# Kernel tuning notes

Hardware: AMD Instinct MI355X
Metric: run time of the kernel (lower is better)

The kernel has to match this reference:

```python
import jax, jax.numpy as jnp
import numpy as np

B, S, D, DEPTH = 2, 2048, 1024, 4
NUM_LEAVES = 2 ** DEPTH          # 16
NUM_DEC = NUM_LEAVES - 1         # 15


def setup_inputs() -> dict:
    key = jax.random.key(0)
    k1, k2, k3, k4, k5 = jax.random.split(key, 5)
    scale = 1.0 / np.sqrt(D)
    return {
        "x": jax.random.normal(k1, (B, S, D), dtype=jnp.float32),
        "dec_w": jax.random.normal(k2, (NUM_DEC, D), dtype=jnp.float32) * scale,
        "dec_b": jax.random.normal(k3, (NUM_DEC,), dtype=jnp.float32) * scale,
        "leaf_w": jax.random.normal(k4, (NUM_LEAVES, D, D), dtype=jnp.float32) * scale,  # [leaf, out, in] (torch Linear layout)
        "leaf_b": jax.random.normal(k5, (NUM_LEAVES, D), dtype=jnp.float32) * scale,
    }


def reference(x, dec_w, dec_b, leaf_w, leaf_b):
    num_leaves = leaf_w.shape[0]
    num_dec = num_leaves - 1
    # All decision-node sigmoids in one batched GEMM: [B,S,num_dec]
    dec = jax.nn.sigmoid(jnp.einsum("bsd,nd->bsn", x, dec_w) + dec_b)
    # Faithful to the original: each tree slot is multiplied exactly once by its
    # direct parent's decision (left child: p, right child: 1-p).
    leaf_idx = np.arange(num_dec, 2 * num_leaves - 1)      # slots holding leaf probs
    parent = (leaf_idx - 1) // 2                           # [num_leaves]
    is_left = (leaf_idx % 2 == 1)                          # [num_leaves]
    dec_p = dec[..., parent]                               # [B,S,num_leaves]
    leaf_probs = jnp.where(jnp.asarray(is_left), dec_p, 1.0 - dec_p)
    # All leaf MLPs as one batched GEMM: [B,S,L,D]
    leaf_out = jnp.einsum("bsd,lod->bslo", x, leaf_w) + leaf_b
    # Probability-weighted sum over leaves -> [B,S,D]
    return jnp.einsum("bslo,bsl->bso", leaf_out, leaf_probs)
```

## Files before the change

kernel.cpp:

```cpp
#include <hip/hip_runtime.h>
#include <stdint.h>


#define M_TOK 4096
#define DDIM  1024
#define KFLAT 9216

typedef __bf16 bf16x8 __attribute__((ext_vector_type(8)));
typedef float  f32x4  __attribute__((ext_vector_type(4)));
typedef unsigned short u16x4 __attribute__((ext_vector_type(4)));
typedef unsigned short u16x8 __attribute__((ext_vector_type(8)));

#define GLB(p) ((const __attribute__((address_space(1))) void*)(p))
#define LDS(p) ((__attribute__((address_space(3))) void*)(p))

__device__ __forceinline__ unsigned short f2bf(float f) {
    union { float f; uint32_t u; } v; v.f = f;
    uint32_t u = v.u;
    return (unsigned short)((u + 0x7fffu + ((u >> 16) & 1u)) >> 16);
}

__device__ __forceinline__ bf16x8 asbf(f32x4 v) {
    bf16x8 r; __builtin_memcpy(&r, &v, 16); return r;
}

template<int OFF>
__device__ __forceinline__ f32x4 dsr(uint32_t a) {
    f32x4 r;
    asm volatile("ds_read_b128 %0, %1 offset:%c2" : "=v"(r) : "v"(a), "i"(OFF));
    return r;
}

__global__ __launch_bounds__(256) void prep_dec_kernel(
    const float* __restrict__ x, const float* __restrict__ dec_w,
    const float* __restrict__ dec_b, const float* __restrict__ lw,
    const float* __restrict__ lb, unsigned short* __restrict__ wp,
    float* __restrict__ bw, unsigned short* __restrict__ xs,
    float* __restrict__ pmat)
{
    if (blockIdx.x < 1024) {
        int idx = blockIdx.x * 256 + threadIdx.x;
        int o  = idx >> 8;
        int k4 = (idx & 255) << 2;
        size_t src = (size_t)o * DDIM + k4;
        size_t dstb = (size_t)o * KFLAT + k4;
        float4 acc = make_float4(0.f, 0.f, 0.f, 0.f);
#pragma unroll
        for (int j = 0; j < 8; ++j) {
            const float4 a = *(const float4*)(lw + (size_t)(2*j)   * DDIM*DDIM + src);
            const float4 b = *(const float4*)(lw + (size_t)(2*j+1) * DDIM*DDIM + src);
            u16x4 d;
            d[0] = f2bf(a.x - b.x); d[1] = f2bf(a.y - b.y);
            d[2] = f2bf(a.z - b.z); d[3] = f2bf(a.w - b.w);
            *(u16x4*)(wp + dstb + (size_t)j * DDIM) = d;
            acc.x += b.x; acc.y += b.y; acc.z += b.z; acc.w += b.w;
        }
        u16x4 s;
        s[0] = f2bf(acc.x); s[1] = f2bf(acc.y); s[2] = f2bf(acc.z); s[3] = f2bf(acc.w);
        *(u16x4*)(wp + dstb + (size_t)8 * DDIM) = s;
        if ((idx & 255) == 0) {
            float sb = 0.f;
#pragma unroll
            for (int j = 0; j < 8; ++j) {
                float ba = lb[(2*j) * DDIM + o];
                float bb = lb[(2*j+1) * DDIM + o];
                bw[j * DDIM + o] = ba - bb;
                sb += bb;
            }
            bw[8 * DDIM + o] = sb;
        }
    } else {
        int m    = (blockIdx.x - 1024) * 4 + (threadIdx.x >> 6);
        int lane = threadIdx.x & 63;
        const float* xr = x + (size_t)m * DDIM + lane * 16;
        float xv[16];
        *(float4*)&xv[0]  = *(const float4*)(xr + 0);
        *(float4*)&xv[4]  = *(const float4*)(xr + 4);
        *(float4*)&xv[8]  = *(const float4*)(xr + 8);
        *(float4*)&xv[12] = *(const float4*)(xr + 12);
        float s[8];
#pragma unroll
        for (int j = 0; j < 8; ++j) {
            const float* wr = dec_w + (size_t)(7 + j) * DDIM + lane * 16;
            float a = 0.f;
#pragma unroll
            for (int i = 0; i < 16; i += 4) {
                float4 wv = *(const float4*)(wr + i);
                a = fmaf(xv[i], wv.x, fmaf(xv[i+1], wv.y, fmaf(xv[i+2], wv.z, fmaf(xv[i+3], wv.w, a))));
            }
            s[j] = a;
        }
#pragma unroll
        for (int j = 0; j < 8; ++j)
#pragma unroll
            for (int off = 32; off > 0; off >>= 1)
                s[j] += __shfl_xor(s[j], off);
        float p[8];
#pragma unroll
        for (int j = 0; j < 8; ++j)
            p[j] = 1.0f / (1.0f + expf(-(s[j] + dec_b[7 + j])));
        if (lane == 0) {
#pragma unroll
            for (int j = 0; j < 8; ++j)
                pmat[(size_t)m * 8 + j] = p[j];
        }
#pragma unroll
        for (int j = 0; j < 9; ++j) {
            float pj = (j < 8) ? p[j] : 1.0f;
            unsigned short* dst = xs + (size_t)m * KFLAT + j * DDIM + lane * 16;
#pragma unroll
            for (int c = 0; c < 2; ++c) {
                u16x8 o;
#pragma unroll
                for (int e = 0; e < 8; ++e) o[e] = f2bf(pj * xv[c * 8 + e]);
                *(u16x8*)(dst + c * 8) = o;
            }
        }
    }
}

#define WAITV0 asm volatile("s_waitcnt vmcnt(0)" ::: "memory")
#define WAITV4 asm volatile("s_waitcnt vmcnt(4)" ::: "memory")
#define WAITV8 asm volatile("s_waitcnt vmcnt(8)" ::: "memory")
#define BARR   __builtin_amdgcn_s_barrier()
#define SBAR   __builtin_amdgcn_sched_barrier(0)
#define LGKM0  do { asm volatile("s_waitcnt lgkmcnt(0)" ::: "memory"); SBAR; } while(0)
#define LGKM4  do { asm volatile("s_waitcnt lgkmcnt(4)" ::: "memory"); SBAR; } while(0)

#define MFMA_Q(q, ASET, BSET) do { \
    __builtin_amdgcn_s_setprio(1); \
    _Pragma("unroll") \
    for (int mfl = 0; mfl < 2; ++mfl) { \
        _Pragma("unroll") \
        for (int j = 0; j < 4; ++j) { \
            acc[2*(q)+mfl][j] = __builtin_amdgcn_mfma_f32_16x16x32_bf16(asbf(ASET[mfl][0]), asbf(BSET[j][0]), acc[2*(q)+mfl][j], 0, 0, 0); \
            acc[2*(q)+mfl][j] = __builtin_amdgcn_mfma_f32_16x16x32_bf16(asbf(ASET[mfl][1]), asbf(BSET[j][1]), acc[2*(q)+mfl][j], 0, 0, 0); \
        } \
    } \
    __builtin_amdgcn_s_setprio(0); \
} while(0)

#define READ_A(SET, q, a0, a1) do { \
    SET[0][0] = dsr<(2*(q)+0)*2048>(a0); \
    SET[0][1] = dsr<(2*(q)+0)*2048>(a1); \
    SET[1][0] = dsr<(2*(q)+1)*2048>(a0); \
    SET[1][1] = dsr<(2*(q)+1)*2048>(a1); \
} while(0)

#define READ_B(SET, b0, b1) do { \
    SET[0][0] = dsr<0*2048>(b0); SET[0][1] = dsr<0*2048>(b1); \
    SET[1][0] = dsr<1*2048>(b0); SET[1][1] = dsr<1*2048>(b1); \
    SET[2][0] = dsr<2*2048>(b0); SET[2][1] = dsr<2*2048>(b1); \
    SET[3][0] = dsr<3*2048>(b0); SET[3][1] = dsr<3*2048>(b1); \
} while(0)

__global__ __launch_bounds__(512, 2) void tree_gemm8(
    const unsigned short* __restrict__ xs, const unsigned short* __restrict__ wp,
    float* __restrict__ out, float* __restrict__ parts, int KG)
{
    extern __shared__ char smem[];
    const int tid  = threadIdx.x;
    const int lane = tid & 63;
    const int w    = tid >> 6;
    const int wm   = w >> 2, wn = w & 3;
    const int ra   = lane & 15;
    const int g16  = lane >> 4;

    const int bx  = blockIdx.x;
    const int xcd = bx & 7, ii = bx >> 3;
    const int nt  = xcd >> 1;
    const int mt  = (xcd & 1) * 8 + ii;
    const int m0  = mt * 256, n0 = nt * 256;
    const int g   = blockIdx.y;
    const int k0  = g * KG;
    const int NT  = KG >> 6;

    uint32_t sbase = (uint32_t)(uintptr_t)(__attribute__((address_space(3))) char*)smem;
    const uint32_t colb0 = (uint32_t)((g16 ^ (ra & 7)) << 4);
    const uint32_t colb1 = colb0 ^ 64;
    const uint32_t baseA0s = sbase + wm * 16384 + ra * 128 + colb0;
    const uint32_t baseA1s = sbase + wm * 16384 + ra * 128 + colb1;
    const uint32_t baseB0s = sbase + 65536 + wn * 8192 + ra * 128 + colb0;
    const uint32_t baseB1s = sbase + 65536 + wn * 8192 + ra * 128 + colb1;

    const int kel = (((lane & 7) ^ (lane >> 3)) & 7) * 8;
    const int rA  = w * 8 + (lane >> 3);

    auto stageA = [&](int buf, int tt, int hh) {
        const unsigned short* s0 = xs + (size_t)(m0 + hh * 128 + rA) * KFLAT + (k0 + tt * 64 + kel);
        char* d0 = smem + buf * 32768 + hh * 16384 + w * 1024;
        __builtin_amdgcn_global_load_lds(GLB(s0), LDS(d0), 16, 0, 0);
        __builtin_amdgcn_global_load_lds(GLB(s0 + (size_t)64 * KFLAT), LDS(d0 + 8192), 16, 0, 0);
    };
    auto stageB = [&](int buf, int tt, int hh) {
        const unsigned short* s0 = wp + (size_t)(n0 + hh * 128 + rA) * KFLAT + (k0 + tt * 64 + kel);
        char* d0 = smem + 65536 + buf * 32768 + hh * 16384 + w * 1024;
        __builtin_amdgcn_global_load_lds(GLB(s0), LDS(d0), 16, 0, 0);
        __builtin_amdgcn_global_load_lds(GLB(s0 + (size_t)64 * KFLAT), LDS(d0 + 8192), 16, 0, 0);
    };

    f32x4 acc[8][4] = {};
    f32x4 avA[2][2], avB[2][2], bvX[4][2], bvY[4][2];

    stageA(0, 0, 0); stageA(0, 0, 1);
    stageB(0, 0, 0); stageB(0, 0, 1);
    stageB(1, 1, 0); stageB(1, 1, 1);
    WAITV4;
    BARR;
    READ_B(bvX, baseB0s, baseB1s);
    READ_A(avA, 0, baseA0s, baseA1s);

    int bt1 = 1, bt2 = 2;

#define TILE_BODY(T, CUR, NXT) do { \
    const int t_ = (T); \
    const bool s1 = (t_ + 1 < NT), s2 = (t_ + 2 < NT); \
    if (s1) { stageA((t_ + 1) & 1, t_ + 1, 0); stageA((t_ + 1) & 1, t_ + 1, 1); } \
    if (s2) { stageB(bt2, t_ + 2, 0); stageB(bt2, t_ + 2, 1); } \
    const uint32_t a0_ = baseA0s + ((uint32_t)(t_ & 1) << 15); \
    const uint32_t a1_ = baseA1s + ((uint32_t)(t_ & 1) << 15); \
    READ_A(avB, 1, a0_, a1_); \
    LGKM4;  MFMA_Q(0, avA, CUR); \
    READ_A(avA, 2, a0_, a1_); \
    LGKM4;  MFMA_Q(1, avB, CUR); \
    READ_A(avB, 3, a0_, a1_); \
    LGKM4;  MFMA_Q(2, avA, CUR); \
    LGKM0; \
    if (s1) { \
        if (s2) { WAITV4; } else { WAITV0; } \
        BARR; \
        const uint32_t nb0_ = baseB0s + (uint32_t)bt1 * 32768u; \
        const uint32_t nb1_ = baseB1s + (uint32_t)bt1 * 32768u; \
        const uint32_t na0_ = baseA0s + ((uint32_t)((t_ + 1) & 1) << 15); \
        const uint32_t na1_ = baseA1s + ((uint32_t)((t_ + 1) & 1) << 15); \
        READ_B(NXT, nb0_, nb1_); \
        READ_A(avA, 0, na0_, na1_); \
    } \
    MFMA_Q(3, avB, CUR); \
    SBAR; \
    bt1 = (bt1 == 2) ? 0 : bt1 + 1; \
    bt2 = (bt2 == 2) ? 0 : bt2 + 1; \
} while(0)

    for (int tp = 0; tp < NT; tp += 2) {
        TILE_BODY(tp,     bvX, bvY);
        TILE_BODY(tp + 1, bvY, bvX);
    }
#undef TILE_BODY

    float* dst = (g == 0) ? out : parts + (size_t)(g - 1) * M_TOK * DDIM;
#pragma unroll
    for (int mf = 0; mf < 8; ++mf)
#pragma unroll
        for (int e = 0; e < 4; ++e) {
            int row = m0 + wm * 128 + mf * 16 + g16 * 4 + e;
#pragma unroll
            for (int j = 0; j < 4; ++j)
                dst[(size_t)row * DDIM + n0 + wn * 64 + j * 16 + ra] = acc[mf][j][e];
        }
}

__global__ __launch_bounds__(256) void reduce2_kernel(
    float* __restrict__ out, const float* __restrict__ parts,
    const float* __restrict__ pmat, const float* __restrict__ bw, int np)
{
    size_t i = (size_t)blockIdx.x * 256 + threadIdx.x;
    int m   = (int)(i >> 8);
    int col = (int)(i & 255) * 4;
    float4 a = ((const float4*)out)[i];
    for (int p = 0; p < np; ++p) {
        float4 b = ((const float4*)(parts + (size_t)p * M_TOK * DDIM))[i];
        a.x += b.x; a.y += b.y; a.z += b.z; a.w += b.w;
    }
    float4 pa = *(const float4*)(pmat + (size_t)m * 8);
    float4 pb = *(const float4*)(pmat + (size_t)m * 8 + 4);
    float4 bias = *(const float4*)(bw + 8 * DDIM + col);
#pragma unroll
    for (int l = 0; l < 8; ++l) {
        float pl = (l < 4) ? ((const float*)&pa)[l] : ((const float*)&pb)[l - 4];
        float4 bl = *(const float4*)(bw + l * DDIM + col);
        bias.x = fmaf(pl, bl.x, bias.x); bias.y = fmaf(pl, bl.y, bias.y);
        bias.z = fmaf(pl, bl.z, bias.z); bias.w = fmaf(pl, bl.w, bias.w);
    }
    a.x += bias.x; a.y += bias.y; a.z += bias.z; a.w += bias.w;
    ((float4*)out)[i] = a;
}

#define MFMA_Q5(q, SET) do { \
    __builtin_amdgcn_s_setprio(1); \
    _Pragma("unroll") \
    for (int mfl = 0; mfl < 2; ++mfl) { \
        _Pragma("unroll") \
        for (int j = 0; j < 4; ++j) { \
            acc[2*(q)+mfl][j] = __builtin_amdgcn_mfma_f32_16x16x32_bf16(asbf(SET[mfl][0]), asbf(bv[j][0]), acc[2*(q)+mfl][j], 0, 0, 0); \
            acc[2*(q)+mfl][j] = __builtin_amdgcn_mfma_f32_16x16x32_bf16(asbf(SET[mfl][1]), asbf(bv[j][1]), acc[2*(q)+mfl][j], 0, 0, 0); \
        } \
    } \
    __builtin_amdgcn_s_setprio(0); \
} while(0)

__global__ __launch_bounds__(512, 2) void tree_gemm5(
    const unsigned short* __restrict__ xs, const unsigned short* __restrict__ wp,
    float* __restrict__ out, float* __restrict__ parts, int KG)
{
    extern __shared__ char smem[];
    const int tid  = threadIdx.x;
    const int lane = tid & 63;
    const int w    = tid >> 6;
    const int wm   = w >> 2, wn = w & 3;
    const int ra   = lane & 15;
    const int g16  = lane >> 4;
    const int bx  = blockIdx.x;
    const int xcd = bx & 7, ii = bx >> 3;
    const int nt  = xcd >> 1;
    const int mt  = (xcd & 1) * 8 + ii;
    const int m0  = mt * 256, n0 = nt * 256;
    const int g   = blockIdx.y;
    const int k0  = g * KG;
    const int NT  = KG >> 6;
    uint32_t sbase = (uint32_t)(uintptr_t)(__attribute__((address_space(3))) char*)smem;
    const uint32_t colb0 = (uint32_t)((g16 ^ (ra & 7)) << 4);
    const uint32_t colb1 = colb0 ^ 64;
    const uint32_t baseA0s = sbase + wm * 16384 + ra * 128 + colb0;
    const uint32_t baseA1s = sbase + wm * 16384 + ra * 128 + colb1;
    const uint32_t baseB0s = sbase + 65536 + wn * 8192 + ra * 128 + colb0;
    const uint32_t baseB1s = sbase + 65536 + wn * 8192 + ra * 128 + colb1;
    const int kel = (((lane & 7) ^ (lane >> 3)) & 7) * 8;
    const int rA  = w * 8 + (lane >> 3);
    auto stageA = [&](int buf, int tt, int hh) {
        const unsigned short* s0 = xs + (size_t)(m0 + hh * 128 + rA) * KFLAT + (k0 + tt * 64 + kel);
        char* d0 = smem + buf * 32768 + hh * 16384 + w * 1024;
        __builtin_amdgcn_global_load_lds(GLB(s0), LDS(d0), 16, 0, 0);
        __builtin_amdgcn_global_load_lds(GLB(s0 + (size_t)64 * KFLAT), LDS(d0 + 8192), 16, 0, 0);
    };
    auto stageB = [&](int buf, int tt, int hh) {
        const unsigned short* s0 = wp + (size_t)(n0 + hh * 128 + rA) * KFLAT + (k0 + tt * 64 + kel);
        char* d0 = smem + 65536 + buf * 32768 + hh * 16384 + w * 1024;
        __builtin_amdgcn_global_load_lds(GLB(s0), LDS(d0), 16, 0, 0);
        __builtin_amdgcn_global_load_lds(GLB(s0 + (size_t)64 * KFLAT), LDS(d0 + 8192), 16, 0, 0);
    };
    f32x4 acc[8][4] = {};
    f32x4 avA[2][2], avB[2][2], bv[4][2];
    stageA(0, 0, 0); stageA(0, 0, 1);
    stageB(0, 0, 0); stageB(0, 0, 1);
    stageA(1, 1, 0); stageA(1, 1, 1);
    stageB(1, 1, 0); stageB(1, 1, 1);
    WAITV8; BARR;
    int bt = 0, bt2 = 2;
    for (int t = 0; t < NT; ++t) {
        if (t) {
            if (t == NT - 1) { WAITV0; } else { WAITV4; }
            BARR;
        }
        if (t + 1 < NT) { stageA((t + 1) & 1, t + 1, 0); stageA((t + 1) & 1, t + 1, 1); }
        if (t + 2 < NT) { stageB(bt2, t + 2, 0); stageB(bt2, t + 2, 1); }
        const uint32_t aoff = (uint32_t)(t & 1) << 15;
        const uint32_t boffv = (uint32_t)bt << 15;
        const uint32_t bA0 = baseA0s + aoff, bA1 = baseA1s + aoff;
        const uint32_t bB0 = baseB0s + boffv, bB1 = baseB1s + boffv;
        READ_B(bv, bB0, bB1);
        READ_A(avA, 0, bA0, bA1);
        READ_A(avB, 1, bA0, bA1);
        LGKM4;  MFMA_Q5(0, avA);
        READ_A(avA, 2, bA0, bA1);
        LGKM4;  MFMA_Q5(1, avB);
        READ_A(avB, 3, bA0, bA1);
        LGKM4;  MFMA_Q5(2, avA);
        LGKM0;  MFMA_Q5(3, avB);
        bt  = (bt  == 2) ? 0 : bt  + 1;
        bt2 = (bt2 == 2) ? 0 : bt2 + 1;
    }
    float* dst = (g == 0) ? out : parts + (size_t)(g - 1) * M_TOK * DDIM;
#pragma unroll
    for (int mf = 0; mf < 8; ++mf)
#pragma unroll
        for (int e = 0; e < 4; ++e) {
            int row = m0 + wm * 128 + mf * 16 + g16 * 4 + e;
#pragma unroll
            for (int j = 0; j < 4; ++j)
                dst[(size_t)row * DDIM + n0 + wn * 64 + j * 16 + ra] = acc[mf][j][e];
        }
}

__global__ __launch_bounds__(256, 4) void tree_gemm3(
    const unsigned short* __restrict__ xs, const unsigned short* __restrict__ wp,
    const float* __restrict__ bw, const float* __restrict__ pmat,
    float* __restrict__ out, float* __restrict__ parts, int KG)
{
    __shared__ __align__(16) unsigned short Asm[2][128 * 32];
    __shared__ __align__(16) unsigned short Bsm[2][128 * 32];
    const int tid  = threadIdx.x;
    const int lane = tid & 63;
    const int w    = tid >> 6;
    const int wm   = w >> 1, wn = w & 1;
    const int bx   = blockIdx.x;
    const int xcd  = bx & 7;
    const int ii   = bx >> 3;
    const int mt   = xcd * 4 + (ii >> 3);
    const int nt   = ii & 7;
    const int m0   = mt * 128, n0 = nt * 128;
    const int g    = blockIdx.y;
    const int k0   = g * KG;
    const int ra   = lane & 15;
    const int kb   = (lane >> 4) * 8;
    f32x4 acc[4][4] = {};
    auto stage = [&](int buf, int t) {
#pragma unroll
        for (int c = 0; c < 2; ++c) {
            int row = w * 32 + c * 16 + (lane >> 2);
            int ke  = k0 + t * 32 + (lane & 3) * 8;
            const unsigned short* ga = xs + (size_t)(m0 + row) * KFLAT + ke;
            __builtin_amdgcn_global_load_lds(GLB(ga), LDS(&Asm[buf][w * 1024 + c * 512]), 16, 0, 0);
            const unsigned short* gb = wp + (size_t)(n0 + row) * KFLAT + ke;
            __builtin_amdgcn_global_load_lds(GLB(gb), LDS(&Bsm[buf][w * 1024 + c * 512]), 16, 0, 0);
        }
    };
    const int TOT = KG >> 5;
    stage(0, 0);
    __syncthreads();
    int cur = 0;
    for (int t = 0; t < TOT; ++t) {
        if (t + 1 < TOT) stage(cur ^ 1, t + 1);
        bf16x8 av2[4], bv2[4];
#pragma unroll
        for (int i2 = 0; i2 < 4; ++i2)
            av2[i2] = *(const bf16x8*)&Asm[cur][(wm * 64 + i2 * 16 + ra) * 32 + kb];
#pragma unroll
        for (int j = 0; j < 4; ++j)
            bv2[j] = *(const bf16x8*)&Bsm[cur][(wn * 64 + j * 16 + ra) * 32 + kb];
#pragma unroll
        for (int i2 = 0; i2 < 4; ++i2)
#pragma unroll
            for (int j = 0; j < 4; ++j)
                acc[i2][j] = __builtin_amdgcn_mfma_f32_16x16x32_bf16(av2[i2], bv2[j], acc[i2][j], 0, 0, 0);
        __syncthreads();
        cur ^= 1;
    }
    float* bsm = (float*)&Asm[0][0];
    if (g == 0) {
        for (int idx = tid; idx < 9 * 128; idx += 256)
            bsm[idx] = bw[(idx >> 7) * DDIM + n0 + (idx & 127)];
    }
    __syncthreads();
    float* dst = (g == 0) ? out : parts + (size_t)(g - 1) * M_TOK * DDIM;
#pragma unroll
    for (int i2 = 0; i2 < 4; ++i2)
#pragma unroll
        for (int r = 0; r < 4; ++r) {
            int row = m0 + wm * 64 + i2 * 16 + (lane >> 4) * 4 + r;
            float4 pa, pb;
            if (g == 0) {
                pa = *(const float4*)(pmat + (size_t)row * 8);
                pb = *(const float4*)(pmat + (size_t)row * 8 + 4);
            }
#pragma unroll
            for (int j = 0; j < 4; ++j) {
                int cl = wn * 64 + j * 16 + ra;
                float v = acc[i2][j][r];
                if (g == 0) {
                    v += pa.x * bsm[0 * 128 + cl] + pa.y * bsm[1 * 128 + cl]
                       + pa.z * bsm[2 * 128 + cl] + pa.w * bsm[3 * 128 + cl]
                       + pb.x * bsm[4 * 128 + cl] + pb.y * bsm[5 * 128 + cl]
                       + pb.z * bsm[6 * 128 + cl] + pb.w * bsm[7 * 128 + cl]
                       + bsm[8 * 128 + cl];
                }
                dst[(size_t)row * DDIM + n0 + cl] = v;
            }
        }
}

__global__ __launch_bounds__(256) void reduce_kernel(
    float* __restrict__ out, const float* __restrict__ parts, int np)
{
    size_t i = (size_t)blockIdx.x * 256 + threadIdx.x;
    float4 a = ((const float4*)out)[i];
    for (int p = 0; p < np; ++p) {
        float4 b = ((const float4*)(parts + (size_t)p * M_TOK * DDIM))[i];
        a.x += b.x; a.y += b.y; a.z += b.z; a.w += b.w;
    }
    ((float4*)out)[i] = a;
}

extern "C" void kernel_launch(void* const* d_in, const int* in_sizes, int n_in,
                              void* d_out, int out_size, void* d_ws, size_t ws_size,
                              hipStream_t stream) {
    (void)in_sizes; (void)n_in; (void)out_size;
    const float* x     = (const float*)d_in[0];
    const float* dec_w = (const float*)d_in[1];
    const float* dec_b = (const float*)d_in[2];
    const float* lw    = (const float*)d_in[3];
    const float* lb    = (const float*)d_in[4];
    float* out = (float*)d_out;
    uint8_t* w8 = (uint8_t*)d_ws;

    unsigned short* xs   = (unsigned short*)(w8);
    unsigned short* wp   = (unsigned short*)(w8 + 75497472);
    float*          bw   = (float*)(w8 + 94371840);
    float*          pmat = (float*)(w8 + 94408704);
    float*          parts= (float*)(w8 + 94539776);
    const size_t NEED3 = 94539776 + 2ull * 16777216;
    const size_t NEED4 = 94539776 + 3ull * 16777216;

    int ks = (ws_size >= NEED4) ? 4 : (ws_size >= NEED3) ? 3 : 0;
    if (!ks) return;

    prep_dec_kernel<<<2048, 256, 0, stream>>>(x, dec_w, dec_b, lw, lb, wp, bw, xs, pmat);

    hipError_t e8 = hipFuncSetAttribute(
        reinterpret_cast<const void*>(tree_gemm8),
        hipFuncAttributeMaxDynamicSharedMemorySize, 163840);
    if (e8 == hipSuccess) {
        tree_gemm8<<<dim3(64, ks), 512, 163840, stream>>>(xs, wp, out, parts, KFLAT / ks);
        reduce2_kernel<<<4096, 256, 0, stream>>>(out, parts, pmat, bw, ks - 1);
        return;
    }
    hipError_t e5 = hipFuncSetAttribute(
        reinterpret_cast<const void*>(tree_gemm5),
        hipFuncAttributeMaxDynamicSharedMemorySize, 163840);
    if (e5 == hipSuccess) {
        tree_gemm5<<<dim3(64, ks), 512, 163840, stream>>>(xs, wp, out, parts, KFLAT / ks);
        reduce2_kernel<<<4096, 256, 0, stream>>>(out, parts, pmat, bw, ks - 1);
    } else {
        tree_gemm3<<<dim3(256, ks), 256, 0, stream>>>(xs, wp, bw, pmat, out, parts, KFLAT / ks);
        reduce_kernel<<<4096, 256, 0, stream>>>(out, parts, ks - 1);
    }
}
```

Baseline: 123.4 us.

## Pre-swizzle weights into MFMA fragment order and load B directly to registers

The prep kernel can now write the folded bf16 weight matrix in a tiled layout that matches each wave's MFMA B-fragment order. A new GEMM kernel then loads B straight from global memory into registers, skipping LDS staging, so shared memory drops to 64 KB with A double-buffered. It also remaps the block index so the K-split groups and N tiles spread across XCDs. This removes LDS traffic and barrier pressure for B, but each wave now fetches its own B fragments from global or L2 with less latency hiding. The tree_gemm5 fallback is removed.

After: 137.2 us. +11.2%, slower.

```diff
diff --git a/kernel.cpp b/kernel.cpp
--- a/kernel.cpp
+++ b/kernel.cpp
@@ -36,14 +36,28 @@
     const float* __restrict__ dec_b, const float* __restrict__ lw,
     const float* __restrict__ lb, unsigned short* __restrict__ wp,
     float* __restrict__ bw, unsigned short* __restrict__ xs,
-    float* __restrict__ pmat)
+    float* __restrict__ pmat, int newlay)
 {
     if (blockIdx.x < 1024) {
         int idx = blockIdx.x * 256 + threadIdx.x;
         int o  = idx >> 8;
         int k4 = (idx & 255) << 2;
         size_t src = (size_t)o * DDIM + k4;
-        size_t dstb = (size_t)o * KFLAT + k4;
+        const int nt = o >> 8, wn = (o >> 6) & 3, jj = (o >> 4) & 3, ra = o & 15;
+        auto store4 = [&](int l, u16x4 d) {
+            if (newlay) {
+                int K    = l * DDIM + k4;
+                int kt   = K >> 6;
+                int half = (K >> 5) & 1;
+                int g16  = (K >> 3) & 3;
+                int e0   = K & 7;
+                size_t a = ((size_t)(nt * 144 + kt) * 4 + wn) * 4096
+                         + (jj * 2 + half) * 512 + (g16 * 16 + ra) * 8 + e0;
+                *(u16x4*)(wp + a) = d;
+            } else {
+                *(u16x4*)(wp + (size_t)o * KFLAT + l * DDIM + k4) = d;
+            }
+        };
         float4 acc = make_float4(0.f, 0.f, 0.f, 0.f);
 #pragma unroll
         for (int j = 0; j < 8; ++j) {
@@ -52,12 +66,12 @@
             u16x4 d;
             d[0] = f2bf(a.x - b.x); d[1] = f2bf(a.y - b.y);
             d[2] = f2bf(a.z - b.z); d[3] = f2bf(a.w - b.w);
-            *(u16x4*)(wp + dstb + (size_t)j * DDIM) = d;
+            store4(j, d);
             acc.x += b.x; acc.y += b.y; acc.z += b.z; acc.w += b.w;
         }
         u16x4 s;
         s[0] = f2bf(acc.x); s[1] = f2bf(acc.y); s[2] = f2bf(acc.z); s[3] = f2bf(acc.w);
-        *(u16x4*)(wp + dstb + (size_t)8 * DDIM) = s;
+        store4(8, s);
         if ((idx & 255) == 0) {
             float sb = 0.f;
 #pragma unroll
@@ -154,6 +168,139 @@
     SET[3][0] = dsr<3*2048>(b0); SET[3][1] = dsr<3*2048>(b1); \
 } while(0)
 
+__global__ __launch_bounds__(512, 2) void tree_gemm9(
+    const unsigned short* __restrict__ xs,
+    const unsigned short* __restrict__ wpf,
+    float* __restrict__ out, float* __restrict__ parts)
+{
+    extern __shared__ char smem[];
+    const int tid  = threadIdx.x;
+    const int lane = tid & 63;
+    const int w    = tid >> 6;
+    const int wm   = w >> 2, wn = w & 3;
+    const int ra   = lane & 15;
+    const int g16  = lane >> 4;
+
+    const int flat = blockIdx.x;
+    const int xcd  = flat & 7;
+    const int idx  = flat >> 3;
+    const int cc   = idx >> 4;
+    const int mt   = idx & 15;
+    const int code = xcd * 2 + cc;
+    const int nt   = code >> 2;
+    const int g    = code & 3;
+    const int m0   = mt * 256, n0 = nt * 256;
+    const int k0   = g * 2304;
+    const int NT   = 36;
+
+    uint32_t sbase = (uint32_t)(uintptr_t)(__attribute__((address_space(3))) char*)smem;
+    const uint32_t colb0 = (uint32_t)((g16 ^ (ra & 7)) << 4);
+    const uint32_t colb1 = colb0 ^ 64;
+    const uint32_t baseA0s = sbase + wm * 16384 + ra * 128 + colb0;
+    const uint32_t baseA1s = sbase + wm * 16384 + ra * 128 + colb1;
+
+    const int kel = (((lane & 7) ^ (lane >> 3)) & 7) * 8;
+    const int rA  = w * 8 + (lane >> 3);
+
+    auto stageA = [&](int buf, int tt, int hh) {
+        const unsigned short* s0 = xs + (size_t)(m0 + hh * 128 + rA) * KFLAT + (k0 + tt * 64 + kel);
+        char* d0 = smem + buf * 32768 + hh * 16384 + w * 1024;
+        __builtin_amdgcn_global_load_lds(GLB(s0), LDS(d0), 16, 0, 0);
+        __builtin_amdgcn_global_load_lds(GLB(s0 + (size_t)64 * KFLAT), LDS(d0 + 8192), 16, 0, 0);
+    };
+
+    const unsigned short* bsrc = wpf
+        + ((size_t)(nt * 144 + g * 36) * 4 + wn) * 4096 + lane * 8;
+
+    f32x4 acc[8][4] = {};
+    f32x4 avA[2][2], avB[2][2], bvX[4][2], bvY[4][2];
+
+    auto loadB = [&](f32x4 (&SET)[4][2], const unsigned short* bp) {
+#pragma unroll
+        for (int j = 0; j < 4; ++j) {
+            SET[j][0] = *(const f32x4*)(bp + (j * 2 + 0) * 512);
+            SET[j][1] = *(const f32x4*)(bp + (j * 2 + 1) * 512);
+        }
+    };
+
+    stageA(0, 0, 0); stageA(0, 0, 1);
+    loadB(bvX, bsrc);
+    WAITV0;
+    BARR;
+    READ_A(avA, 0, baseA0s, baseA1s);
+
+#define TILE_BODY(T, CUR, NXT) do { \
+    const int t_ = (T); \
+    const bool s1 = (t_ + 1 < NT); \
+    if (s1) { \
+        stageA((t_ + 1) & 1, t_ + 1, 0); stageA((t_ + 1) & 1, t_ + 1, 1); \
+        loadB(NXT, bsrc + 16384); \
+    } \
+    const uint32_t a0_ = baseA0s + ((uint32_t)(t_ & 1) << 15); \
+    const uint32_t a1_ = baseA1s + ((uint32_t)(t_ & 1) << 15); \
+    READ_A(avB, 1, a0_, a1_); \
+    LGKM4;  MFMA_Q(0, avA, CUR); \
+    READ_A(avA, 2, a0_, a1_); \
+    LGKM4;  MFMA_Q(1, avB, CUR); \
+    READ_A(avB, 3, a0_, a1_); \
+    LGKM4;  MFMA_Q(2, avA, CUR); \
+    LGKM0; \
+    if (s1) { \
+        WAITV0; \
+        BARR; \
+        const uint32_t na0_ = baseA0s + ((uint32_t)((t_ + 1) & 1) << 15); \
+        const uint32_t na1_ = baseA1s + ((uint32_t)((t_ + 1) & 1) << 15); \
+        READ_A(avA, 0, na0_, na1_); \
+    } \
+    MFMA_Q(3, avB, CUR); \
+    SBAR; \
+    bsrc += 16384; \
+} while(0)
+
+    for (int tp = 0; tp < NT; tp += 2) {
+        TILE_BODY(tp,     bvX, bvY);
+        TILE_BODY(tp + 1, bvY, bvX);
+    }
+#undef TILE_BODY
+
+    float* dst = (g == 0) ? out : parts + (size_t)(g - 1) * M_TOK * DDIM;
+#pragma unroll
+    for (int mf = 0; mf < 8; ++mf)
+#pragma unroll
+        for (int e = 0; e < 4; ++e) {
+            int row = m0 + wm * 128 + mf * 16 + g16 * 4 + e;
+#pragma unroll
+            for (int j = 0; j < 4; ++j)
+                dst[(size_t)row * DDIM + n0 + wn * 64 + j * 16 + ra] = acc[mf][j][e];
+        }
+}
+
+__global__ __launch_bounds__(256) void reduce2_kernel(
+    float* __restrict__ out, const float* __restrict__ parts,
+    const float* __restrict__ pmat, const float* __restrict__ bw, int np)
+{
+    size_t i = (size_t)blockIdx.x * 256 + threadIdx.x;
+    int m   = (int)(i >> 8);
+    int col = (int)(i & 255) * 4;
+    float4 a = ((const float4*)out)[i];
+    for (int p = 0; p < np; ++p) {
+        float4 b = ((const float4*)(parts + (size_t)p * M_TOK * DDIM))[i];
+        a.x += b.x; a.y += b.y; a.z += b.z; a.w += b.w;
+    }
+    float4 pa = *(const float4*)(pmat + (size_t)m * 8);
+    float4 pb = *(const float4*)(pmat + (size_t)m * 8 + 4);
+    float4 bias = *(const float4*)(bw + 8 * DDIM + col);
+#pragma unroll
+    for (int l = 0; l < 8; ++l) {
+        float pl = (l < 4) ? ((const float*)&pa)[l] : ((const float*)&pb)[l - 4];
+        float4 bl = *(const float4*)(bw + l * DDIM + col);
+        bias.x = fmaf(pl, bl.x, bias.x); bias.y = fmaf(pl, bl.y, bias.y);
+        bias.z = fmaf(pl, bl.z, bias.z); bias.w = fmaf(pl, bl.w, bias.w);
+    }
+    a.x += bias.x; a.y += bias.y; a.z += bias.z; a.w += bias.w;
+    ((float4*)out)[i] = a;
+}
+
 __global__ __launch_bounds__(512, 2) void tree_gemm8(
     const unsigned short* __restrict__ xs, const unsigned short* __restrict__ wp,
     float* __restrict__ out, float* __restrict__ parts, int KG)
@@ -212,7 +359,7 @@
 
     int bt1 = 1, bt2 = 2;
 
-#define TILE_BODY(T, CUR, NXT) do { \
+#define TILE_BODY8(T, CUR, NXT) do { \
     const int t_ = (T); \
     const bool s1 = (t_ + 1 < NT), s2 = (t_ + 2 < NT); \
     if (s1) { stageA((t_ + 1) & 1, t_ + 1, 0); stageA((t_ + 1) & 1, t_ + 1, 1); } \
@@ -243,133 +390,11 @@
 } while(0)
 
     for (int tp = 0; tp < NT; tp += 2) {
-        TILE_BODY(tp,     bvX, bvY);
-        TILE_BODY(tp + 1, bvY, bvX);
-    }
-#undef TILE_BODY
-
-    float* dst = (g == 0) ? out : parts + (size_t)(g - 1) * M_TOK * DDIM;
-#pragma unroll
-    for (int mf = 0; mf < 8; ++mf)
-#pragma unroll
-        for (int e = 0; e < 4; ++e) {
-            int row = m0 + wm * 128 + mf * 16 + g16 * 4 + e;
-#pragma unroll
-            for (int j = 0; j < 4; ++j)
-                dst[(size_t)row * DDIM + n0 + wn * 64 + j * 16 + ra] = acc[mf][j][e];
-        }
-}
-
-__global__ __launch_bounds__(256) void reduce2_kernel(
-    float* __restrict__ out, const float* __restrict__ parts,
-    const float* __restrict__ pmat, const float* __restrict__ bw, int np)
-{
-    size_t i = (size_t)blockIdx.x * 256 + threadIdx.x;
-    int m   = (int)(i >> 8);
-    int col = (int)(i & 255) * 4;
-    float4 a = ((const float4*)out)[i];
-    for (int p = 0; p < np; ++p) {
-        float4 b = ((const float4*)(parts + (size_t)p * M_TOK * DDIM))[i];
-        a.x += b.x; a.y += b.y; a.z += b.z; a.w += b.w;
-    }
-    float4 pa = *(const float4*)(pmat + (size_t)m * 8);
-    float4 pb = *(const float4*)(pmat + (size_t)m * 8 + 4);
-    float4 bias = *(const float4*)(bw + 8 * DDIM + col);
-#pragma unroll
-    for (int l = 0; l < 8; ++l) {
-        float pl = (l < 4) ? ((const float*)&pa)[l] : ((const float*)&pb)[l - 4];
-        float4 bl = *(const float4*)(bw + l * DDIM + col);
-        bias.x = fmaf(pl, bl.x, bias.x); bias.y = fmaf(pl, bl.y, bias.y);
-        bias.z = fmaf(pl, bl.z, bias.z); bias.w = fmaf(pl, bl.w, bias.w);
-    }
-    a.x += bias.x; a.y += bias.y; a.z += bias.z; a.w += bias.w;
-    ((float4*)out)[i] = a;
-}
-
-#define MFMA_Q5(q, SET) do { \
-    __builtin_amdgcn_s_setprio(1); \
-    _Pragma("unroll") \
-    for (int mfl = 0; mfl < 2; ++mfl) { \
-        _Pragma("unroll") \
-        for (int j = 0; j < 4; ++j) { \
-            acc[2*(q)+mfl][j] = __builtin_amdgcn_mfma_f32_16x16x32_bf16(asbf(SET[mfl][0]), asbf(bv[j][0]), acc[2*(q)+mfl][j], 0, 0, 0); \
-            acc[2*(q)+mfl][j] = __builtin_amdgcn_mfma_f32_16x16x32_bf16(asbf(SET[mfl][1]), asbf(bv[j][1]), acc[2*(q)+mfl][j], 0, 0, 0); \
-        } \
-    } \
-    __builtin_amdgcn_s_setprio(0); \
-} while(0)
-
-__global__ __launch_bounds__(512, 2) void tree_gemm5(
-    const unsigned short* __restrict__ xs, const unsigned short* __restrict__ wp,
-    float* __restrict__ out, float* __restrict__ parts, int KG)
-{
-    extern __shared__ char smem[];
-    const int tid  = threadIdx.x;
-    const int lane = tid & 63;
-    const int w    = tid >> 6;
-    const int wm   = w >> 2, wn = w & 3;
-    const int ra   = lane & 15;
-    const int g16  = lane >> 4;
-    const int bx  = blockIdx.x;
-    const int xcd = bx & 7, ii = bx >> 3;
-    const int nt  = xcd >> 1;
-    const int mt  = (xcd & 1) * 8 + ii;
-    const int m0  = mt * 256, n0 = nt * 256;
-    const int g   = blockIdx.y;
-    const int k0  = g * KG;
-    const int NT  = KG >> 6;
-    uint32_t sbase = (uint32_t)(uintptr_t)(__attribute__((address_space(3))) char*)smem;
-    const uint32_t colb0 = (uint32_t)((g16 ^ (ra & 7)) << 4);
-    const uint32_t colb1 = colb0 ^ 64;
-    const uint32_t baseA0s = sbase + wm * 16384 + ra * 128 + colb0;
-    const uint32_t baseA1s = sbase + wm * 16384 + ra * 128 + colb1;
-    const uint32_t baseB0s = sbase + 65536 + wn * 8192 + ra * 128 + colb0;
-    const uint32_t baseB1s = sbase + 65536 + wn * 8192 + ra * 128 + colb1;
-    const int kel = (((lane & 7) ^ (lane >> 3)) & 7) * 8;
-    const int rA  = w * 8 + (lane >> 3);
-    auto stageA = [&](int buf, int tt, int hh) {
-        const unsigned short* s0 = xs + (size_t)(m0 + hh * 128 + rA) * KFLAT + (k0 + tt * 64 + kel);
-        char* d0 = smem + buf * 32768 + hh * 16384 + w * 1024;
-        __builtin_amdgcn_global_load_lds(GLB(s0), LDS(d0), 16, 0, 0);
-        __builtin_amdgcn_global_load_lds(GLB(s0 + (size_t)64 * KFLAT), LDS(d0 + 8192), 16, 0, 0);
-    };
-    auto stageB = [&](int buf, int tt, int hh) {
-        const unsigned short* s0 = wp + (size_t)(n0 + hh * 128 + rA) * KFLAT + (k0 + tt * 64 + kel);
-        char* d0 = smem + 65536 + buf * 32768 + hh * 16384 + w * 1024;
-        __builtin_amdgcn_global_load_lds(GLB(s0), LDS(d0), 16, 0, 0);
-        __builtin_amdgcn_global_load_lds(GLB(s0 + (size_t)64 * KFLAT), LDS(d0 + 8192), 16, 0, 0);
-    };
-    f32x4 acc[8][4] = {};
-    f32x4 avA[2][2], avB[2][2], bv[4][2];
-    stageA(0, 0, 0); stageA(0, 0, 1);
-    stageB(0, 0, 0); stageB(0, 0, 1);
-    stageA(1, 1, 0); stageA(1, 1, 1);
-    stageB(1, 1, 0); stageB(1, 1, 1);
-    WAITV8; BARR;
-    int bt = 0, bt2 = 2;
-    for (int t = 0; t < NT; ++t) {
-        if (t) {
-            if (t == NT - 1) { WAITV0; } else { WAITV4; }
-            BARR;
-        }
-        if (t + 1 < NT) { stageA((t + 1) & 1, t + 1, 0); stageA((t + 1) & 1, t + 1, 1); }
-        if (t + 2 < NT) { stageB(bt2, t + 2, 0); stageB(bt2, t + 2, 1); }
-        const uint32_t aoff = (uint32_t)(t & 1) << 15;
-        const uint32_t boffv = (uint32_t)bt << 15;
-        const uint32_t bA0 = baseA0s + aoff, bA1 = baseA1s + aoff;
-        const uint32_t bB0 = baseB0s + boffv, bB1 = baseB1s + boffv;
-        READ_B(bv, bB0, bB1);
-        READ_A(avA, 0, bA0, bA1);
-        READ_A(avB, 1, bA0, bA1);
-        LGKM4;  MFMA_Q5(0, avA);
-        READ_A(avA, 2, bA0, bA1);
-        LGKM4;  MFMA_Q5(1, avB);
-        READ_A(avB, 3, bA0, bA1);
-        LGKM4;  MFMA_Q5(2, avA);
-        LGKM0;  MFMA_Q5(3, avB);
-        bt  = (bt  == 2) ? 0 : bt  + 1;
-        bt2 = (bt2 == 2) ? 0 : bt2 + 1;
-    }
+        TILE_BODY8(tp,     bvX, bvY);
+        TILE_BODY8(tp + 1, bvY, bvX);
+    }
+#undef TILE_BODY8
+
     float* dst = (g == 0) ? out : parts + (size_t)(g - 1) * M_TOK * DDIM;
 #pragma unroll
     for (int mf = 0; mf < 8; ++mf)
@@ -504,7 +529,22 @@
     int ks = (ws_size >= NEED4) ? 4 : (ws_size >= NEED3) ? 3 : 0;
     if (!ks) return;
 
-    prep_dec_kernel<<<2048, 256, 0, stream>>>(x, dec_w, dec_b, lw, lb, wp, bw, xs, pmat);
+    bool use9 = false;
+    if (ks == 4) {
+        hipError_t e9 = hipFuncSetAttribute(
+            reinterpret_cast<const void*>(tree_gemm9),
+            hipFuncAttributeMaxDynamicSharedMemorySize, 65536);
+        use9 = (e9 == hipSuccess);
+    }
+
+    prep_dec_kernel<<<2048, 256, 0, stream>>>(x, dec_w, dec_b, lw, lb, wp, bw, xs, pmat,
+                                              use9 ? 1 : 0);
+
+    if (use9) {
+        tree_gemm9<<<256, 512, 65536, stream>>>(xs, wp, out, parts);
+        reduce2_kernel<<<4096, 256, 0, stream>>>(out, parts, pmat, bw, 3);
+        return;
+    }
 
     hipError_t e8 = hipFuncSetAttribute(
         reinterpret_cast<const void*>(tree_gemm8),
@@ -512,14 +552,6 @@
     if (e8 == hipSuccess) {
         tree_gemm8<<<dim3(64, ks), 512, 163840, stream>>>(xs, wp, out, parts, KFLAT / ks);
         reduce2_kernel<<<4096, 256, 0, stream>>>(out, parts, pmat, bw, ks - 1);
-        return;
-    }
-    hipError_t e5 = hipFuncSetAttribute(
-        reinterpret_cast<const void*>(tree_gemm5),
-        hipFuncAttributeMaxDynamicSharedMemorySize, 163840);
-    if (e5 == hipSuccess) {
-        tree_gemm5<<<dim3(64, ks), 512, 163840, stream>>>(xs, wp, out, parts, KFLAT / ks);
-        reduce2_kernel<<<4096, 256, 0, stream>>>(out, parts, pmat, bw, ks - 1);
     } else {
         tree_gemm3<<<dim3(256, ks), 256, 0, stream>>>(xs, wp, bw, pmat, out, parts, KFLAT / ks);
         reduce_kernel<<<4096, 256, 0, stream>>>(out, parts, ks - 1);
```
